# Kernel tuning notes

Measured on AMD Instinct MI355X. Metric: run time of the kernel, lower is better.

The kernel has to match this reference:

```python
import jax, jax.numpy as jnp
import numpy as np

EPS = 1e-8  # torch.cosine_similarity default eps


def setup_inputs() -> dict:
    key = jax.random.key(0)
    ks = jax.random.split(key, 6)
    B, S, H, D = 512, 4096, 32, 16
    return {
        "decoder_hidden_final_layer": jax.random.normal(ks[0], (B, H), dtype=jnp.float32),
        "encoder_outputs": jax.random.normal(ks[1], (B, S, H), dtype=jnp.float32),
        "Wq": jax.random.normal(ks[2], (D, H), dtype=jnp.float32) * 0.1,
        "bq": jax.random.normal(ks[3], (D,), dtype=jnp.float32) * 0.1,
        "Wk": jax.random.normal(ks[4], (D, H), dtype=jnp.float32) * 0.1,
        "bk": jax.random.normal(ks[5], (D,), dtype=jnp.float32) * 0.1,
    }


def reference(decoder_hidden_final_layer, encoder_outputs, Wq, bq, Wk, bk):
    # q projection of encoder outputs: [B,S,D]; k projection of decoder state: [B,D]
    q = jnp.einsum("bsh,dh->bsd", encoder_outputs, Wq) + bq
    k = decoder_hidden_final_layer @ Wk.T + bk
    # cosine similarity: normalize once, then a single contraction (same math as
    # torch.cosine_similarity with eps clamp on the norms)
    qn = q / jnp.maximum(jnp.linalg.norm(q, axis=-1, keepdims=True), EPS)
    kn = k / jnp.maximum(jnp.linalg.norm(k, axis=-1, keepdims=True), EPS)
    attention = jnp.einsum("bsd,bd->bs", qn, kn)  # [B,S]
    weightings = jax.nn.log_softmax(attention, axis=1)  # softmax over S (torch dim=1)
    return weightings[:, None, :]  # transpose(1,2): [B,1,S]
```

## Files before the change

### kernel.cpp

```cpp
#include <hip/hip_runtime.h>
#include <math.h>

#define BB    512
#define SS    4096
#define HH    32
#define DD    16
#define NT    256
#define CHUNK 256
#define NCH   (SS / CHUNK)
#define TILES (CHUNK / 16)
#define TPW   (TILES / 4)
#define EPSI  1e-8f

typedef __attribute__((ext_vector_type(8))) short   short8;
typedef __attribute__((ext_vector_type(4))) float   floatx4;

__device__ __forceinline__ short bf16_of(float f) {
    union { float f; unsigned u; } v; v.f = f;
    return (short)((v.u + 0x7FFFu + ((v.u >> 16) & 1u)) >> 16);
}

template <int CTRL>
__device__ __forceinline__ float dpp_add(float x) {
    int xi = __builtin_bit_cast(int, x);
    int yi = __builtin_amdgcn_update_dpp(0, xi, CTRL, 0xF, 0xF, true);
    return x + __builtin_bit_cast(float, yi);
}
__device__ __forceinline__ float red16(float x) {
    x = dpp_add<0xB1>(x);
    x = dpp_add<0x4E>(x);
    x = dpp_add<0x141>(x);
    x = dpp_add<0x140>(x);
    return x;
}

__global__ __launch_bounds__(NT, 2)
void attn_cos_logsoftmax(const float* __restrict__ dec,
                         const float* __restrict__ enc,
                         const float* __restrict__ Wq,
                         const float* __restrict__ bq,
                         const float* __restrict__ Wk,
                         const float* __restrict__ bk,
                         float* __restrict__ out)
{
    __shared__ short encS[2][CHUNK * HH];
    __shared__ float attS[SS];
    __shared__ float knS[DD];
    __shared__ float redM[4], redS[4];

    const int t    = threadIdx.x;
    const int b    = blockIdx.x;
    const int lane = t & 63;
    const int wv   = t >> 6;
    const int l15  = lane & 15;
    const int quad = lane >> 4;

    const float4* encb4 = (const float4*)(enc + (size_t)b * SS * HH);

    float4 pf[8];
#pragma unroll
    for (int i = 0; i < 8; ++i) pf[i] = encb4[i * NT + t];

    short8 bfrag;
    {
        const float* wp = Wq + l15 * HH + quad * 8;
        float4 w0 = *(const float4*)wp;
        float4 w1 = *(const float4*)(wp + 4);
        bfrag[0] = bf16_of(w0.x); bfrag[1] = bf16_of(w0.y);
        bfrag[2] = bf16_of(w0.z); bfrag[3] = bf16_of(w0.w);
        bfrag[4] = bf16_of(w1.x); bfrag[5] = bf16_of(w1.y);
        bfrag[6] = bf16_of(w1.z); bfrag[7] = bf16_of(w1.w);
    }

    const float bqV = bq[l15];

    {
        float dh[HH];
#pragma unroll
        for (int h = 0; h < HH; ++h) dh[h] = dec[b * HH + h];
        float kacc[DD], ssk = 0.f;
#pragma unroll
        for (int d = 0; d < DD; ++d) {
            float a = bk[d];
#pragma unroll
            for (int h = 0; h < HH; ++h) a = fmaf(Wk[d * HH + h], dh[h], a);
            kacc[d] = a; ssk = fmaf(a, a, ssk);
        }
        float inv = 1.f / fmaxf(sqrtf(ssk), EPSI);
        if (t == 0) {
#pragma unroll
            for (int d = 0; d < DD; ++d) knS[d] = kacc[d] * inv;
        }
    }
    __syncthreads();
    const float knV = knS[l15];

    for (int c = 0; c < NCH; ++c) {
        short* dst = encS[c & 1];
#pragma unroll
        for (int i = 0; i < 8; ++i) {
            union { short s[4]; unsigned long long u; } pk;
            pk.s[0] = bf16_of(pf[i].x); pk.s[1] = bf16_of(pf[i].y);
            pk.s[2] = bf16_of(pf[i].z); pk.s[3] = bf16_of(pf[i].w);
            *(unsigned long long*)&dst[(i * NT + t) * 4] = pk.u;
        }
        if (c + 1 < NCH) {
            const float4* src = encb4 + (size_t)(c + 1) * (CHUNK * HH / 4);
#pragma unroll
            for (int i = 0; i < 8; ++i) pf[i] = src[i * NT + t];
        }
        __syncthreads();

        const short* sbuf = encS[c & 1];
        const int cbase = c * CHUNK;
#pragma unroll
        for (int i2 = 0; i2 < TPW; ++i2) {
            const int tile = wv * TPW + i2;
            short8 afrag = *(const short8*)&sbuf[(tile * 16 + l15) * HH + quad * 8];
            floatx4 acc = {0.f, 0.f, 0.f, 0.f};
            acc = __builtin_amdgcn_mfma_f32_16x16x32_bf16(afrag, bfrag, acc, 0, 0, 0);
            float4 av;
            float* avp = &av.x;
#pragma unroll
            for (int r = 0; r < 4; ++r) {
                float qv = acc[r] + bqV;
                float ss = red16(qv * qv);
                float nu = red16(qv * knV);
                avp[r] = nu / fmaxf(sqrtf(ss), EPSI);
            }
            if (l15 == 0)
                *(float4*)&attS[cbase + tile * 16 + quad * 4] = av;
        }
    }
    __syncthreads();

    float m = -INFINITY;
#pragma unroll
    for (int i = 0; i < 16; ++i) m = fmaxf(m, attS[t + i * NT]);
#pragma unroll
    for (int off = 32; off >= 1; off >>= 1) m = fmaxf(m, __shfl_down(m, off));
    if (lane == 0) redM[wv] = m;
    __syncthreads();
    const float M = fmaxf(fmaxf(redM[0], redM[1]), fmaxf(redM[2], redM[3]));

    float s = 0.f;
#pragma unroll
    for (int i = 0; i < 16; ++i) s += __expf(attS[t + i * NT] - M);
#pragma unroll
    for (int off = 32; off >= 1; off >>= 1) s += __shfl_down(s, off);
    if (lane == 0) redS[wv] = s;
    __syncthreads();
    const float S = (redS[0] + redS[1]) + (redS[2] + redS[3]);
    const float logZ = M + __logf(S);

    float4* ob4 = (float4*)(out + (size_t)b * SS);
#pragma unroll
    for (int i = 0; i < 4; ++i) {
        float4 a4 = *(const float4*)&attS[(t + i * NT) * 4];
        a4.x -= logZ; a4.y -= logZ; a4.z -= logZ; a4.w -= logZ;
        ob4[t + i * NT] = a4;
    }
}

extern "C" void kernel_launch(void* const* d_in, const int* in_sizes, int n_in,
                              void* d_out, int out_size, void* d_ws, size_t ws_size,
                              hipStream_t stream) {
    const float* dec = (const float*)d_in[0];
    const float* enc = (const float*)d_in[1];
    const float* Wq  = (const float*)d_in[2];
    const float* bq  = (const float*)d_in[3];
    const float* Wk  = (const float*)d_in[4];
    const float* bk  = (const float*)d_in[5];
    float* out = (float*)d_out;

    attn_cos_logsoftmax<<<dim3(BB), dim3(NT), 0, stream>>>(dec, enc, Wq, bq, Wk, bk, out);
}
```

Before: 379.5 us.

## Load MFMA fragments directly from global per wave, dropping LDS staging

Each wave now owns a contiguous quarter of the sequence and loads its bf16 A fragments straight from global memory into registers, using a 4-deep register prefetch ring. This replaces the block-wide LDS double buffer and its per-chunk __syncthreads. The k projection is also computed per lane with a 16-lane DPP reduction instead of one thread writing to shared memory. The goal is to remove LDS round trips and barriers from a bandwidth-bound stream. The cost is per-lane 32-byte strided global loads, which may coalesce worse than the previous fully contiguous float4 pattern.

```diff
diff --git a/kernel.cpp b/kernel.cpp
--- a/kernel.cpp
+++ b/kernel.cpp
@@ -6,10 +6,11 @@
 #define HH    32
 #define DD    16
 #define NT    256
-#define CHUNK 256
-#define NCH   (SS / CHUNK)
-#define TILES (CHUNK / 16)
-#define TPW   (TILES / 4)
+#define WAVES 4
+#define RPW   (SS / WAVES)
+#define TPW   (RPW / 16)
+#define DEPTH 4
+#define NGRP  (TPW / DEPTH)
 #define EPSI  1e-8f
 
 typedef __attribute__((ext_vector_type(8))) short   short8;
@@ -43,10 +44,8 @@
                          const float* __restrict__ bk,
                          float* __restrict__ out)
 {
-    __shared__ short encS[2][CHUNK * HH];
     __shared__ float attS[SS];
-    __shared__ float knS[DD];
-    __shared__ float redM[4], redS[4];
+    __shared__ float redM[WAVES], redS[WAVES];
 
     const int t    = threadIdx.x;
     const int b    = blockIdx.x;
@@ -55,11 +54,18 @@
     const int l15  = lane & 15;
     const int quad = lane >> 4;
 
-    const float4* encb4 = (const float4*)(enc + (size_t)b * SS * HH);
+    const float* encb = enc + (size_t)b * SS * HH;
+    const int rowbase = wv * RPW;
 
-    float4 pf[8];
+    const float* src0 = encb + (size_t)(rowbase + l15) * HH + quad * 8;
+
+    float4 pf[DEPTH][2];
 #pragma unroll
-    for (int i = 0; i < 8; ++i) pf[i] = encb4[i * NT + t];
+    for (int s = 0; s < DEPTH; ++s) {
+        const float* p = src0 + (size_t)s * 16 * HH;
+        pf[s][0] = *(const float4*)p;
+        pf[s][1] = *(const float4*)(p + 4);
+    }
 
     short8 bfrag;
     {
@@ -71,56 +77,40 @@
         bfrag[4] = bf16_of(w1.x); bfrag[5] = bf16_of(w1.y);
         bfrag[6] = bf16_of(w1.z); bfrag[7] = bf16_of(w1.w);
     }
-
     const float bqV = bq[l15];
 
+    float knV;
     {
-        float dh[HH];
+        float a = bk[l15];
+        const float* wk = Wk + l15 * HH;
 #pragma unroll
-        for (int h = 0; h < HH; ++h) dh[h] = dec[b * HH + h];
-        float kacc[DD], ssk = 0.f;
+        for (int h = 0; h < HH; ++h) a = fmaf(wk[h], dec[b * HH + h], a);
+        float ssk = red16(a * a);
+        knV = a * (1.f / fmaxf(sqrtf(ssk), EPSI));
+    }
+
+    float* attW = attS + rowbase;
+    for (int g = 0; g < NGRP; ++g) {
 #pragma unroll
-        for (int d = 0; d < DD; ++d) {
-            float a = bk[d];
-#pragma unroll
-            for (int h = 0; h < HH; ++h) a = fmaf(Wk[d * HH + h], dh[h], a);
-            kacc[d] = a; ssk = fmaf(a, a, ssk);
-        }
-        float inv = 1.f / fmaxf(sqrtf(ssk), EPSI);
-        if (t == 0) {
-#pragma unroll
-            for (int d = 0; d < DD; ++d) knS[d] = kacc[d] * inv;
-        }
-    }
-    __syncthreads();
-    const float knV = knS[l15];
+        for (int s = 0; s < DEPTH; ++s) {
+            const int i = g * DEPTH + s;
+            float4 p0 = pf[s][0];
+            float4 p1 = pf[s][1];
+            if (g + 1 < NGRP) {
+                const float* p = src0 + (size_t)(i + DEPTH) * 16 * HH;
+                pf[s][0] = *(const float4*)p;
+                pf[s][1] = *(const float4*)(p + 4);
+            }
+            short8 afrag;
+            afrag[0] = bf16_of(p0.x); afrag[1] = bf16_of(p0.y);
+            afrag[2] = bf16_of(p0.z); afrag[3] = bf16_of(p0.w);
+            afrag[4] = bf16_of(p1.x); afrag[5] = bf16_of(p1.y);
+            afrag[6] = bf16_of(p1.z); afrag[7] = bf16_of(p1.w);
 
-    for (int c = 0; c < NCH; ++c) {
-        short* dst = encS[c & 1];
-#pragma unroll
-        for (int i = 0; i < 8; ++i) {
-            union { short s[4]; unsigned long long u; } pk;
-            pk.s[0] = bf16_of(pf[i].x); pk.s[1] = bf16_of(pf[i].y);
-            pk.s[2] = bf16_of(pf[i].z); pk.s[3] = bf16_of(pf[i].w);
-            *(unsigned long long*)&dst[(i * NT + t) * 4] = pk.u;
-        }
-        if (c + 1 < NCH) {
-            const float4* src = encb4 + (size_t)(c + 1) * (CHUNK * HH / 4);
-#pragma unroll
-            for (int i = 0; i < 8; ++i) pf[i] = src[i * NT + t];
-        }
-        __syncthreads();
-
-        const short* sbuf = encS[c & 1];
-        const int cbase = c * CHUNK;
-#pragma unroll
-        for (int i2 = 0; i2 < TPW; ++i2) {
-            const int tile = wv * TPW + i2;
-            short8 afrag = *(const short8*)&sbuf[(tile * 16 + l15) * HH + quad * 8];
             floatx4 acc = {0.f, 0.f, 0.f, 0.f};
             acc = __builtin_amdgcn_mfma_f32_16x16x32_bf16(afrag, bfrag, acc, 0, 0, 0);
-            float4 av;
-            float* avp = &av.x;
+
+            float4 av; float* avp = &av.x;
 #pragma unroll
             for (int r = 0; r < 4; ++r) {
                 float qv = acc[r] + bqV;
@@ -129,7 +119,7 @@
                 avp[r] = nu / fmaxf(sqrtf(ss), EPSI);
             }
             if (l15 == 0)
-                *(float4*)&attS[cbase + tile * 16 + quad * 4] = av;
+                *(float4*)&attW[i * 16 + quad * 4] = av;
         }
     }
     __syncthreads();
```

New measurement: 376.2 us. Within noise of the previous version (-0.9%).
